# Kernel optimization log

Hardware: AMD Instinct MI355X
Metric: run time of the kernel (lower is better)

The kernel has to match this reference:

```python
import jax, jax.numpy as jnp
import numpy as np

E = 262144   # number of half-edges / feature rows
C = 128      # in_channels
K = 4        # neighbors per half-edge
O = 256      # out_channels


def setup_inputs() -> dict:
    key = jax.random.key(0)
    k1, k2, k3, k4 = jax.random.split(key, 4)
    x = jax.random.normal(k1, (E, C), dtype=jnp.float32)
    neighbor_idx = jax.random.randint(k2, (E, K), 0, E, dtype=jnp.int64)
    W = jax.random.normal(k3, (K * C, O), dtype=jnp.float32) / np.sqrt(K * C)
    b = jax.random.normal(k4, (O,), dtype=jnp.float32) * 0.01
    return {"x": x, "neighbor_idx": neighbor_idx, "W": W, "b": b}


def reference(x, neighbor_idx, W, b):
    # gather neighbor features: [E, K, C] -> concat -> [E, K*C]
    gathered = x[neighbor_idx].reshape(x.shape[0], -1)
    # Linear + ReLU, batched over all half-edges
    out = jnp.maximum(gathered @ W + b, 0.0)
    return out
```

## Files before the change

kernel.cpp:

```cpp
#include <hip/hip_runtime.h>
#include <hip/hip_bf16.h>


#define E_ROWS 262144
#define C_IN   128
#define KN     4
#define O_OUT  256
#define BM     128
#define BN     128
#define BK     32
#define NSTEPS 16
#define NT     256

typedef __attribute__((ext_vector_type(8))) short bf16x8;
typedef __attribute__((ext_vector_type(4))) float f32x4;

__device__ __forceinline__ unsigned short bf16_rne(float f) {
    unsigned u = __float_as_uint(f);
    return (unsigned short)((u + 0x7fffu + ((u >> 16) & 1u)) >> 16);
}

__global__ void prep_w(const float* __restrict__ W, uint4* __restrict__ wimg) {
    __shared__ float Ws[32][260];
    const int s = blockIdx.x;
    const int t = threadIdx.x;
    #pragma unroll
    for (int i = 0; i < 8; ++i) {
        int v4 = i * 256 + t;
        int k  = v4 >> 6;
        int n4 = v4 & 63;
        float4 w = ((const float4*)W)[(size_t)(s * 32 + k) * 64 + n4];
        *(float4*)&Ws[k][n4 * 4] = w;
    }
    __syncthreads();
    #pragma unroll
    for (int i = 0; i < 8; ++i) {
        int q  = i * 256 + t;
        int nb = q >> 10;
        int h  = (q >> 9) & 1;
        int cl = q & 511;
        int nl = cl >> 2;
        int cs = cl & 3;
        int c  = cs ^ ((nl >> 1) & 3);
        int n  = nb * 128 + nl;
        int kb = c * 8;
        unsigned short v[8];
        #pragma unroll
        for (int e = 0; e < 8; ++e) {
            float w = Ws[kb + e][n];
            unsigned u  = __float_as_uint(w);
            unsigned hb = (u + 0x7fffu + ((u >> 16) & 1u)) & 0xffff0000u;
            float r = w - __uint_as_float(hb);
            v[e] = h ? bf16_rne(r) : (unsigned short)(hb >> 16);
        }
        uint4 o;
        o.x = (unsigned)v[0] | ((unsigned)v[1] << 16);
        o.y = (unsigned)v[2] | ((unsigned)v[3] << 16);
        o.z = (unsigned)v[4] | ((unsigned)v[5] << 16);
        o.w = (unsigned)v[6] | ((unsigned)v[7] << 16);
        wimg[(size_t)nb * 16384 + (size_t)(2 * s + h) * 512 + cl] = o;
    }
}

__global__ __launch_bounds__(NT, 4) void gemm(
    const float* __restrict__ x,
    const int* __restrict__ nidx,
    const uint4* __restrict__ wimg,
    const float* __restrict__ bias,
    float* __restrict__ out)
{
    __shared__ __align__(16) float A_s[BM * BK];
    __shared__ __align__(16) unsigned short B_s[2 * BN * BK];
    __shared__ int   idx_s[BM * KN];
    __shared__ float b_s[BN];

    const int t  = threadIdx.x;
    const int m0 = blockIdx.x * BM;
    const int nb = blockIdx.y;
    const int n0 = nb * BN;

    idx_s[t]       = nidx[(size_t)m0 * KN + t];
    idx_s[t + 256] = nidx[(size_t)m0 * KN + 256 + t];
    if (t < BN) b_s[t] = bias[n0 + t];

    const int l   = t & 63;
    const int wid = t >> 6;
    const int wm  = wid >> 1;
    const int wn  = wid & 1;
    const int lr  = l & 15;
    const int lg  = l >> 4;

    int arow[4], ac[4];
    #pragma unroll
    for (int i = 0; i < 4; ++i) {
        int q   = t + 256 * i;
        arow[i] = q >> 3;
        ac[i]   = (q & 7) ^ (arow[i] & 7);
    }

    const uint4* wbase = wimg + (size_t)nb * 16384;

    f32x4 acc[4][4];
    #pragma unroll
    for (int i = 0; i < 4; ++i)
        #pragma unroll
        for (int jj = 0; jj < 4; ++jj)
            acc[i][jj] = (f32x4){0.f, 0.f, 0.f, 0.f};

    char* Abase = (char*)&A_s[0];
    char* Bbase = (char*)&B_s[0];

    __syncthreads();

    #pragma unroll 1
    for (int s = 0; s < NSTEPS; ++s) {
        const int j  = s >> 2;
        const int kc = (s & 3) << 5;

        #pragma unroll
        for (int i = 0; i < 4; ++i) {
            const float* src = x + (size_t)idx_s[arow[i] * KN + j] * C_IN + kc + (ac[i] << 2);
            __builtin_amdgcn_global_load_lds(
                (const __attribute__((address_space(1))) void*)src,
                (__attribute__((address_space(3))) void*)(Abase + (i << 12) + (wid << 10)),
                16, 0, 0);
        }
        #pragma unroll
        for (int i = 0; i < 2; ++i) {
            const uint4* srcH = wbase + (size_t)(2 * s) * 512 + (t + 256 * i);
            const uint4* srcL = wbase + (size_t)(2 * s + 1) * 512 + (t + 256 * i);
            __builtin_amdgcn_global_load_lds(
                (const __attribute__((address_space(1))) void*)srcH,
                (__attribute__((address_space(3))) void*)(Bbase + (i << 12) + (wid << 10)),
                16, 0, 0);
            __builtin_amdgcn_global_load_lds(
                (const __attribute__((address_space(1))) void*)srcL,
                (__attribute__((address_space(3))) void*)(Bbase + 8192 + (i << 12) + (wid << 10)),
                16, 0, 0);
        }
        __syncthreads();

        bf16x8 bh[4], bl[4];
        #pragma unroll
        for (int nf = 0; nf < 4; ++nf) {
            int nl  = (wn << 6) + (nf << 4) + lr;
            int cB  = lg ^ ((nl >> 1) & 3);
            int off = nl * 64 + cB * 16;
            bh[nf] = *(const bf16x8*)(Bbase + off);
            bl[nf] = *(const bf16x8*)(Bbase + 8192 + off);
        }

        #pragma unroll
        for (int mf = 0; mf < 4; ++mf) {
            int row = (wm << 6) + (mf << 4) + lr;
            int c0  = (lg << 1) ^ (lr & 7);
            f32x4 a0 = *(const f32x4*)(Abase + row * 128 + c0 * 16);
            f32x4 a1 = *(const f32x4*)(Abase + row * 128 + (c0 ^ 1) * 16);
            float av[8];
            av[0]=a0[0]; av[1]=a0[1]; av[2]=a0[2]; av[3]=a0[3];
            av[4]=a1[0]; av[5]=a1[1]; av[6]=a1[2]; av[7]=a1[3];
            bf16x8 ah, al;
            #pragma unroll
            for (int e = 0; e < 8; ++e) {
                unsigned u  = __float_as_uint(av[e]);
                unsigned hb = u & 0xffff0000u;
                ah[e] = (short)(u >> 16);
                al[e] = (short)bf16_rne(av[e] - __uint_as_float(hb));
            }
            #pragma unroll
            for (int nf = 0; nf < 4; ++nf) {
                acc[mf][nf] = __builtin_amdgcn_mfma_f32_16x16x32_bf16(ah, bh[nf], acc[mf][nf], 0, 0, 0);
                acc[mf][nf] = __builtin_amdgcn_mfma_f32_16x16x32_bf16(ah, bl[nf], acc[mf][nf], 0, 0, 0);
                acc[mf][nf] = __builtin_amdgcn_mfma_f32_16x16x32_bf16(al, bh[nf], acc[mf][nf], 0, 0, 0);
            }
        }
        __syncthreads();
    }

    #pragma unroll
    for (int mf = 0; mf < 4; ++mf) {
        #pragma unroll
        for (int nf = 0; nf < 4; ++nf) {
            int colL = (wn << 6) + (nf << 4) + lr;
            int col  = n0 + colL;
            float bv = b_s[colL];
            int rowb = m0 + (wm << 6) + (mf << 4) + (lg << 2);
            #pragma unroll
            for (int r = 0; r < 4; ++r) {
                float v = acc[mf][nf][r] + bv;
                out[(size_t)(rowb + r) * O_OUT + col] = fmaxf(v, 0.f);
            }
        }
    }
}

extern "C" void kernel_launch(void* const* d_in, const int* in_sizes, int n_in,
                              void* d_out, int out_size, void* d_ws, size_t ws_size,
                              hipStream_t stream) {
    const float* x    = (const float*)d_in[0];
    const int*   nidx = (const int*)d_in[1];
    const float* W    = (const float*)d_in[2];
    const float* bias = (const float*)d_in[3];
    float* out  = (float*)d_out;
    uint4* wimg = (uint4*)d_ws;

    hipLaunchKernelGGL(prep_w, dim3(NSTEPS), dim3(256), 0, stream, W, wimg);
    hipLaunchKernelGGL(gemm, dim3(E_ROWS / BM, O_OUT / BN), dim3(NT), 0, stream,
                       x, nidx, wimg, bias, out);
}
```

Baseline: 610.6 us.

## Double-buffer LDS tiles and use 512 threads with smaller per-warp M tile

Doubles the A and B shared-memory buffers so the async global-to-LDS loads for the next K-step are issued before computing the current one, overlapping the gathered x loads with MFMA work. The block grows to 512 threads (8 waves), and each wave now owns 32 rows instead of 64, which halves accumulator registers per thread. LDS use per block doubles (about 66KB), which may cut blocks per CU, and each wave reloads the same B fragments, so B-to-register traffic relative to MFMA work doubles. The launch-bounds occupancy hint is left unchanged at 4 while the block size doubles.

```diff
diff --git a/kernel.cpp b/kernel.cpp
--- a/kernel.cpp
+++ b/kernel.cpp
@@ -10,7 +10,7 @@
 #define BN     128
 #define BK     32
 #define NSTEPS 16
-#define NT     256
+#define NT     512
 
 typedef __attribute__((ext_vector_type(8))) short bf16x8;
 typedef __attribute__((ext_vector_type(4))) float f32x4;
@@ -69,8 +69,8 @@
     const float* __restrict__ bias,
     float* __restrict__ out)
 {
-    __shared__ __align__(16) float A_s[BM * BK];
-    __shared__ __align__(16) unsigned short B_s[2 * BN * BK];
+    __shared__ __align__(16) float A_s[2][BM * BK];
+    __shared__ __align__(16) unsigned short B_s[2][2 * BN * BK];
     __shared__ int   idx_s[BM * KN];
     __shared__ float b_s[BN];
 
@@ -79,8 +79,7 @@
     const int nb = blockIdx.y;
     const int n0 = nb * BN;
 
-    idx_s[t]       = nidx[(size_t)m0 * KN + t];
-    idx_s[t + 256] = nidx[(size_t)m0 * KN + 256 + t];
+    idx_s[t] = nidx[(size_t)m0 * KN + t];
     if (t < BN) b_s[t] = bias[n0 + t];
 
     const int l   = t & 63;
@@ -90,72 +89,64 @@
     const int lr  = l & 15;
     const int lg  = l >> 4;
 
-    int arow[4], ac[4];
-    #pragma unroll
-    for (int i = 0; i < 4; ++i) {
-        int q   = t + 256 * i;
-        arow[i] = q >> 3;
-        ac[i]   = (q & 7) ^ (arow[i] & 7);
-    }
+    const int arow0 = t >> 3;
+    const int ac0   = (t & 7) ^ (arow0 & 7);
+    const int arow1 = (512 + t) >> 3;
+    const int ac1   = ((512 + t) & 7) ^ (arow1 & 7);
 
     const uint4* wbase = wimg + (size_t)nb * 16384;
 
-    f32x4 acc[4][4];
-    #pragma unroll
-    for (int i = 0; i < 4; ++i)
+    f32x4 acc[2][4];
+    #pragma unroll
+    for (int i = 0; i < 2; ++i)
         #pragma unroll
         for (int jj = 0; jj < 4; ++jj)
             acc[i][jj] = (f32x4){0.f, 0.f, 0.f, 0.f};
 
-    char* Abase = (char*)&A_s[0];
-    char* Bbase = (char*)&B_s[0];
-
-    __syncthreads();
-
-    #pragma unroll 1
-    for (int s = 0; s < NSTEPS; ++s) {
+    char* Aall = (char*)&A_s[0][0];
+    char* Ball = (char*)&B_s[0][0];
+
+    auto STAGE = [&](int s, int buf) {
         const int j  = s >> 2;
         const int kc = (s & 3) << 5;
-
-        #pragma unroll
-        for (int i = 0; i < 4; ++i) {
-            const float* src = x + (size_t)idx_s[arow[i] * KN + j] * C_IN + kc + (ac[i] << 2);
-            __builtin_amdgcn_global_load_lds(
-                (const __attribute__((address_space(1))) void*)src,
-                (__attribute__((address_space(3))) void*)(Abase + (i << 12) + (wid << 10)),
-                16, 0, 0);
-        }
-        #pragma unroll
-        for (int i = 0; i < 2; ++i) {
-            const uint4* srcH = wbase + (size_t)(2 * s) * 512 + (t + 256 * i);
-            const uint4* srcL = wbase + (size_t)(2 * s + 1) * 512 + (t + 256 * i);
-            __builtin_amdgcn_global_load_lds(
-                (const __attribute__((address_space(1))) void*)srcH,
-                (__attribute__((address_space(3))) void*)(Bbase + (i << 12) + (wid << 10)),
-                16, 0, 0);
-            __builtin_amdgcn_global_load_lds(
-                (const __attribute__((address_space(1))) void*)srcL,
-                (__attribute__((address_space(3))) void*)(Bbase + 8192 + (i << 12) + (wid << 10)),
-                16, 0, 0);
-        }
-        __syncthreads();
-
+        char* Ab = Aall + (buf << 14);
+        char* Bb = Ball + (buf << 14);
+        const float* a0p = x + (size_t)idx_s[arow0 * KN + j] * C_IN + kc + (ac0 << 2);
+        const float* a1p = x + (size_t)idx_s[arow1 * KN + j] * C_IN + kc + (ac1 << 2);
+        __builtin_amdgcn_global_load_lds(
+            (const __attribute__((address_space(1))) void*)a0p,
+            (__attribute__((address_space(3))) void*)(Ab + (wid << 10)), 16, 0, 0);
+        __builtin_amdgcn_global_load_lds(
+            (const __attribute__((address_space(1))) void*)a1p,
+            (__attribute__((address_space(3))) void*)(Ab + 8192 + (wid << 10)), 16, 0, 0);
+        const uint4* sH = wbase + (size_t)(2 * s) * 512 + t;
+        const uint4* sL = wbase + (size_t)(2 * s + 1) * 512 + t;
+        __builtin_amdgcn_global_load_lds(
+            (const __attribute__((address_space(1))) void*)sH,
+            (__attribute__((address_space(3))) void*)(Bb + (wid << 10)), 16, 0, 0);
+        __builtin_amdgcn_global_load_lds(
+            (const __attribute__((address_space(1))) void*)sL,
+            (__attribute__((address_space(3))) void*)(Bb + 8192 + (wid << 10)), 16, 0, 0);
+    };
+
+    auto COMPUTE = [&](int buf) {
+        char* Ab = Aall + (buf << 14);
+        char* Bb = Ball + (buf << 14);
         bf16x8 bh[4], bl[4];
         #pragma unroll
         for (int nf = 0; nf < 4; ++nf) {
             int nl  = (wn << 6) + (nf << 4) + lr;
             int cB  = lg ^ ((nl >> 1) & 3);
             int off = nl * 64 + cB * 16;
-            bh[nf] = *(const bf16x8*)(Bbase + off);
-            bl[nf] = *(const bf16x8*)(Bbase + 8192 + off);
-        }
-
-        #pragma unroll
-        for (int mf = 0; mf < 4; ++mf) {
-            int row = (wm << 6) + (mf << 4) + lr;
-            int c0  = (lg << 1) ^ (lr & 7);
-            f32x4 a0 = *(const f32x4*)(Abase + row * 128 + c0 * 16);
-            f32x4 a1 = *(const f32x4*)(Abase + row * 128 + (c0 ^ 1) * 16);
+            bh[nf] = *(const bf16x8*)(Bb + off);
+            bl[nf] = *(const bf16x8*)(Bb + 8192 + off);
+        }
+        #pragma unroll
+        for (int mf = 0; mf < 2; ++mf) {
+            int row = (wm << 5) + (mf << 4) + lr;
+            int c0  = (lg << 1) ^ (row & 7);
+            f32x4 a0 = *(const f32x4*)(Ab + row * 128 + c0 * 16);
+            f32x4 a1 = *(const f32x4*)(Ab + row * 128 + (c0 ^ 1) * 16);
             float av[8];
             av[0]=a0[0]; av[1]=a0[1]; av[2]=a0[2]; av[3]=a0[3];
             av[4]=a1[0]; av[5]=a1[1]; av[6]=a1[2]; av[7]=a1[3];
@@ -174,17 +165,30 @@
                 acc[mf][nf] = __builtin_amdgcn_mfma_f32_16x16x32_bf16(al, bh[nf], acc[mf][nf], 0, 0, 0);
             }
         }
+    };
+
+    __syncthreads();
+    STAGE(0, 0);
+    __syncthreads();
+
+    #pragma unroll 1
+    for (int s = 0; s < NSTEPS; s += 2) {
+        if (s + 1 < NSTEPS) STAGE(s + 1, 1);
+        COMPUTE(0);
         __syncthreads();
-    }
-
-    #pragma unroll
-    for (int mf = 0; mf < 4; ++mf) {
+        if (s + 2 < NSTEPS) STAGE(s + 2, 0);
+        COMPUTE(1);
+        __syncthreads();
+    }
+
+    #pragma unroll
+    for (int mf = 0; mf < 2; ++mf) {
         #pragma unroll
         for (int nf = 0; nf < 4; ++nf) {
             int colL = (wn << 6) + (nf << 4) + lr;
             int col  = n0 + colL;
             float bv = b_s[colL];
-            int rowb = m0 + (wm << 6) + (mf << 4) + (lg << 2);
+            int rowb = m0 + (wm << 5) + (mf << 4) + (lg << 2);
             #pragma unroll
             for (int r = 0; r < 4; ++r) {
                 float v = acc[mf][nf][r] + bv;
```

Measured after the change: 543.1 us. -11.1%, faster.
